# Optimization experiments

Measured on AMD Instinct MI355X. Metric: run time of the kernel, lower is better.

The kernel has to match this reference:

```python
import jax, jax.numpy as jnp
import numpy as np

B = 4            # batch size (max batch index + 1, fixed by construction)
H, W = 176, 200  # feature_map_size; x in [0,H), y in [0,W)
C_IN, C_OUT = 128, 256
BW, N = 4096, 64
EPS = 1e-5       # torch LayerNorm default


def setup_inputs() -> dict:
    key = jax.random.key(0)
    k1, k2, k3, k4, k5, k6, k7 = jax.random.split(key, 7)
    window_features = jax.random.normal(k1, (BW, N, C_IN), jnp.float32)
    bidx = jax.random.randint(k2, (BW, N, 1), 0, B)
    xidx = jax.random.randint(k3, (BW, N, 1), -8, H + 8)   # includes invalid coords
    yidx = jax.random.randint(k4, (BW, N, 1), -8, W + 8)
    window_indices = jnp.concatenate([bidx, xidx, yidx], axis=-1).astype(jnp.int32)
    norm_weight = 1.0 + 0.1 * jax.random.normal(k5, (C_IN,), jnp.float32)
    norm_bias = 0.1 * jax.random.normal(k6, (C_IN,), jnp.float32)
    lin_weight = jax.random.normal(k7, (C_OUT, C_IN), jnp.float32) / np.sqrt(C_IN)
    return {"window_features": window_features, "window_indices": window_indices,
            "norm_weight": norm_weight, "norm_bias": norm_bias, "lin_weight": lin_weight}


def reference(window_features, window_indices, norm_weight, norm_bias, lin_weight):
    # window_features: (BW, N, C_IN); window_indices: (BW, N, 3) = (batch, x, y)
    bw, n, c = window_features.shape
    feats = window_features.reshape(-1, c)                # (P, C)
    idx = window_indices.reshape(-1, 3)
    b, x, y = idx[:, 0], idx[:, 1], idx[:, 2]
    valid = (x >= 0) & (x < H) & (y >= 0) & (y < W)

    # unique + index_add_ + sparse-to-dense == scatter-add into dense BEV grid.
    # Invalid rows are routed out-of-bounds and dropped.
    bs = jnp.where(valid, b, B)
    xs = jnp.where(valid, x, 0)
    ys = jnp.where(valid, y, 0)
    # dense layout matches spconv: spatial_shape=[W, H], indices (b, y, x)
    dense_sum = jnp.zeros((B, W, H, c), window_features.dtype)
    dense_sum = dense_sum.at[bs, ys, xs].add(feats, mode="drop")
    count = jnp.zeros((B, W, H), window_features.dtype)
    count = count.at[bs, ys, xs].add(1.0, mode="drop")
    occupied = count > 0                                   # cells holding a unique voxel

    # LayerNorm over C (patch_norm=True) then Linear (bias=False) on occupied cells
    mu = jnp.mean(dense_sum, axis=-1, keepdims=True)
    var = jnp.mean(jnp.square(dense_sum - mu), axis=-1, keepdims=True)
    normed = (dense_sum - mu) * jax.lax.rsqrt(var + EPS) * norm_weight + norm_bias
    dense_out = jnp.einsum("bwhc,oc->bwho", normed, lin_weight)
    dense_out = jnp.where(occupied[..., None], dense_out, 0.0)  # empty cells stay zero

    # gather_operation: pull dense features back to each valid window point
    gathered = dense_out[jnp.where(valid, b, 0), ys, xs]   # (P, C_OUT)
    new_feats = jnp.where(valid[:, None], gathered, 0.0).reshape(bw, n, C_OUT)
    return new_feats, window_indices
```

## Files before the change

kernel.cpp:

```cpp
#include <hip/hip_runtime.h>
#include <stdint.h>

#define HH 176
#define WW 200
#define BB 4
#define CIN 128
#define COUT 256
#define NPTS (4096 * 64)
#define CELLS (BB * WW * HH)
#define FEAT_OUT_ELEMS ((size_t)NPTS * COUT)
#define CAP 32
#define LDSW16 260
#define FLATCAP 1024

typedef __attribute__((ext_vector_type(8))) short bf16x8;
typedef __attribute__((ext_vector_type(4))) float f32x4;

__device__ __forceinline__ unsigned short f2bf(float f) {
    union { float f; unsigned int u; } c; c.f = f;
    unsigned int u = c.u;
    u += 0x7fffu + ((u >> 16) & 1u);
    return (unsigned short)(u >> 16);
}
__device__ __forceinline__ float bf2f(unsigned int h16) {
    union { unsigned int u; float f; } c; c.u = h16 << 16;
    return c.f;
}

__global__ __launch_bounds__(256) void build_kernel(
    const int* __restrict__ idx, int* __restrict__ counts, int* __restrict__ plist,
    float* __restrict__ out_idx, float* __restrict__ out_feats)
{
    __shared__ unsigned char validf[256];
    int tid = threadIdx.x;
    int p0 = blockIdx.x * 256;
    int p = p0 + tid;
    int b = idx[3 * p], x = idx[3 * p + 1], y = idx[3 * p + 2];
    out_idx[3 * p]     = (float)b;
    out_idx[3 * p + 1] = (float)x;
    out_idx[3 * p + 2] = (float)y;
    bool valid = ((unsigned)x < HH && (unsigned)y < WW);
    validf[tid] = valid ? 1 : 0;
    if (valid) {
        int cell = (b * WW + y) * HH + x;
        int slot = atomicAdd(&counts[cell], 1);
        if (slot < CAP) plist[(size_t)cell * CAP + slot] = p;
    }
    __syncthreads();
    int w = tid >> 6, lane = tid & 63;
    float4 z = { 0.0f, 0.0f, 0.0f, 0.0f };
    for (int v = w; v < 256; v += 4)
        if (!validf[v])
            *(float4*)(out_feats + (size_t)(p0 + v) * COUT + lane * 4) = z;
}

__global__ __launch_bounds__(256) void cell_kernel(
    const float* __restrict__ feats, const int* __restrict__ counts,
    const int* __restrict__ plist,
    const float* __restrict__ nw, const float* __restrict__ nb,
    unsigned short* __restrict__ normed)
{
    int cell = blockIdx.x * 4 + (threadIdx.x >> 6);
    int lane = threadIdx.x & 63;
    int n = counts[cell]; n = n < CAP ? n : CAP;
    const int* pl = plist + (size_t)cell * CAP;
    float a0 = 0.0f, a1 = 0.0f;
    for (int i = 0; i < n; ++i) {
        int pid = pl[i];
        float2 v = *(const float2*)(feats + (size_t)pid * CIN + lane * 2);
        a0 += v.x; a1 += v.y;
    }
    float s = a0 + a1;
    float ss = a0 * a0 + a1 * a1;
    #pragma unroll
    for (int m = 32; m >= 1; m >>= 1) {
        s  += __shfl_xor(s, m, 64);
        ss += __shfl_xor(ss, m, 64);
    }
    float mu  = s * (1.0f / 128.0f);
    float var = ss * (1.0f / 128.0f) - mu * mu;
    float inv = rsqrtf(var + 1e-5f);
    float w0 = nw[lane * 2], w1 = nw[lane * 2 + 1];
    float b0 = nb[lane * 2], b1 = nb[lane * 2 + 1];
    ushort2 st;
    st.x = f2bf((a0 - mu) * inv * w0 + b0);
    st.y = f2bf((a1 - mu) * inv * w1 + b1);
    *(ushort2*)(normed + (size_t)cell * CIN + lane * 2) = st;
}

__global__ __launch_bounds__(256) void wcvt_kernel(
    const float* __restrict__ lw, unsigned short* __restrict__ wb)
{
    int i = blockIdx.x * 256 + threadIdx.x;
    wb[i] = f2bf(lw[i]);
}

__global__ __launch_bounds__(256) void gemm_scatter_kernel(
    const unsigned short* __restrict__ A,
    const unsigned short* __restrict__ Wb,
    const int* __restrict__ counts,
    const int* __restrict__ plist,
    float* __restrict__ out)
{
    __shared__ unsigned short lds16[64 * LDSW16];
    __shared__ int fpid[FLATCAP];
    __shared__ unsigned char fcell[FLATCAP];
    __shared__ int nflat;

    int n0 = blockIdx.x * 64;
    int tid = threadIdx.x;
    int w = tid >> 6;
    int lane = tid & 63;
    int l15 = lane & 15;
    int kgrp = (lane >> 4) * 8;
    int orow = (lane >> 4) * 4;

    if (tid == 0) nflat = 0;
    __syncthreads();

    if (tid < 64) {
        int cnt = counts[n0 + tid]; cnt = cnt < CAP ? cnt : CAP;
        if (cnt > 0) {
            int base = atomicAdd(&nflat, cnt);
            for (int s = 0; s < cnt; ++s) {
                int pos = base + s;
                if (pos < FLATCAP) {
                    fpid[pos] = plist[(size_t)(n0 + tid) * CAP + s];
                    fcell[pos] = (unsigned char)tid;
                }
            }
        }
    }

    bf16x8 a[4][4];
    #pragma unroll
    for (int i = 0; i < 4; ++i)
        #pragma unroll
        for (int kk = 0; kk < 4; ++kk)
            a[i][kk] = *(const bf16x8*)(Wb + (size_t)(((w * 4 + i) * 16 + l15) * CIN) + kgrp + kk * 32);

    const unsigned short* bbase = A + (size_t)(n0 + l15) * CIN + kgrp;

    #pragma unroll
    for (int j = 0; j < 4; ++j) {
        bf16x8 bb[4];
        #pragma unroll
        for (int kk = 0; kk < 4; ++kk)
            bb[kk] = *(const bf16x8*)(bbase + (size_t)j * 16 * CIN + kk * 32);

        f32x4 acc[4];
        #pragma unroll
        for (int i = 0; i < 4; ++i) acc[i] = (f32x4){0.0f, 0.0f, 0.0f, 0.0f};
        #pragma unroll
        for (int kk = 0; kk < 4; ++kk)
            #pragma unroll
            for (int i = 0; i < 4; ++i)
                acc[i] = __builtin_amdgcn_mfma_f32_16x16x32_bf16(a[i][kk], bb[kk], acc[i], 0, 0, 0);

        #pragma unroll
        for (int i = 0; i < 4; ++i) {
            int o = (w * 4 + i) * 16 + orow;
            ushort4 st;
            st.x = f2bf(acc[i][0]);
            st.y = f2bf(acc[i][1]);
            st.z = f2bf(acc[i][2]);
            st.w = f2bf(acc[i][3]);
            *(ushort4*)(&lds16[(j * 16 + l15) * LDSW16 + o]) = st;
        }
    }

    __syncthreads();

    int nt = nflat; nt = nt < FLATCAP ? nt : FLATCAP;
    for (int k = w; k < nt; k += 4) {
        int pid = fpid[k];
        int c = fcell[k];
        ushort4 v = *(const ushort4*)(&lds16[c * LDSW16 + lane * 4]);
        float4 o4;
        o4.x = bf2f(v.x);
        o4.y = bf2f(v.y);
        o4.z = bf2f(v.z);
        o4.w = bf2f(v.w);
        *(float4*)(out + (size_t)pid * COUT + lane * 4) = o4;
    }
}

extern "C" void kernel_launch(void* const* d_in, const int* in_sizes, int n_in,
                              void* d_out, int out_size, void* d_ws, size_t ws_size,
                              hipStream_t stream)
{
    const float* feats = (const float*)d_in[0];
    const int*   idx   = (const int*)d_in[1];
    const float* nw    = (const float*)d_in[2];
    const float* nb    = (const float*)d_in[3];
    const float* lw    = (const float*)d_in[4];
    float* out = (float*)d_out;

    char* ws = (char*)d_ws;
    int* counts = (int*)ws;
    int* plist  = (int*)(ws + (1u << 20));
    unsigned short* normed = (unsigned short*)(ws + (20u << 20));
    unsigned short* wb     = (unsigned short*)(ws + (60u << 20));

    hipMemsetAsync(counts, 0, (size_t)CELLS * 4, stream);
    build_kernel<<<NPTS / 256, 256, 0, stream>>>(idx, counts, plist, out + FEAT_OUT_ELEMS, out);
    cell_kernel<<<CELLS / 4, 256, 0, stream>>>(feats, counts, plist, nw, nb, normed);
    wcvt_kernel<<<COUT * CIN / 256, 256, 0, stream>>>(lw, wb);
    gemm_scatter_kernel<<<CELLS / 64, 256, 0, stream>>>(normed, wb, counts, plist, out);
}
```

Measured before the change: 478.2 us.

## Fuse per-cell accumulation and LayerNorm into GEMM-scatter kernel with LDS staging

```diff
diff --git a/kernel.cpp b/kernel.cpp
--- a/kernel.cpp
+++ b/kernel.cpp
@@ -10,6 +10,8 @@
 #define CELLS (BB * WW * HH)
 #define FEAT_OUT_ELEMS ((size_t)NPTS * COUT)
 #define CAP 32
+#define TCELLS 32
+#define LDSWF 132
 #define LDSW16 260
 #define FLATCAP 1024
 
@@ -25,6 +27,15 @@
 __device__ __forceinline__ float bf2f(unsigned int h16) {
     union { unsigned int u; float f; } c; c.u = h16 << 16;
     return c.f;
+}
+
+__global__ __launch_bounds__(256) void prep_kernel(
+    const float* __restrict__ lw, unsigned short* __restrict__ wb,
+    int* __restrict__ counts)
+{
+    int i = blockIdx.x * 256 + threadIdx.x;
+    if (i < COUT * CIN) wb[i] = f2bf(lw[i]);
+    counts[i] = 0;
 }
 
 __global__ __launch_bounds__(256) void build_kernel(
@@ -54,81 +65,68 @@
             *(float4*)(out_feats + (size_t)(p0 + v) * COUT + lane * 4) = z;
 }
 
-__global__ __launch_bounds__(256) void cell_kernel(
-    const float* __restrict__ feats, const int* __restrict__ counts,
-    const int* __restrict__ plist,
-    const float* __restrict__ nw, const float* __restrict__ nb,
-    unsigned short* __restrict__ normed)
-{
-    int cell = blockIdx.x * 4 + (threadIdx.x >> 6);
-    int lane = threadIdx.x & 63;
-    int n = counts[cell]; n = n < CAP ? n : CAP;
-    const int* pl = plist + (size_t)cell * CAP;
-    float a0 = 0.0f, a1 = 0.0f;
-    for (int i = 0; i < n; ++i) {
-        int pid = pl[i];
-        float2 v = *(const float2*)(feats + (size_t)pid * CIN + lane * 2);
-        a0 += v.x; a1 += v.y;
-    }
-    float s = a0 + a1;
-    float ss = a0 * a0 + a1 * a1;
-    #pragma unroll
-    for (int m = 32; m >= 1; m >>= 1) {
-        s  += __shfl_xor(s, m, 64);
-        ss += __shfl_xor(ss, m, 64);
-    }
-    float mu  = s * (1.0f / 128.0f);
-    float var = ss * (1.0f / 128.0f) - mu * mu;
-    float inv = rsqrtf(var + 1e-5f);
-    float w0 = nw[lane * 2], w1 = nw[lane * 2 + 1];
-    float b0 = nb[lane * 2], b1 = nb[lane * 2 + 1];
-    ushort2 st;
-    st.x = f2bf((a0 - mu) * inv * w0 + b0);
-    st.y = f2bf((a1 - mu) * inv * w1 + b1);
-    *(ushort2*)(normed + (size_t)cell * CIN + lane * 2) = st;
-}
-
-__global__ __launch_bounds__(256) void wcvt_kernel(
-    const float* __restrict__ lw, unsigned short* __restrict__ wb)
-{
-    int i = blockIdx.x * 256 + threadIdx.x;
-    wb[i] = f2bf(lw[i]);
-}
-
-__global__ __launch_bounds__(256) void gemm_scatter_kernel(
-    const unsigned short* __restrict__ A,
+__global__ __launch_bounds__(256) void fused_kernel(
+    const float* __restrict__ feats,
     const unsigned short* __restrict__ Wb,
     const int* __restrict__ counts,
     const int* __restrict__ plist,
+    const float* __restrict__ nw, const float* __restrict__ nb,
     float* __restrict__ out)
 {
-    __shared__ unsigned short lds16[64 * LDSW16];
+    __shared__ float accf[TCELLS * LDSWF];
+    __shared__ unsigned short normedl[TCELLS * LDSWF];
     __shared__ int fpid[FLATCAP];
     __shared__ unsigned char fcell[FLATCAP];
+    __shared__ int scnt[TCELLS];
     __shared__ int nflat;
-
-    int n0 = blockIdx.x * 64;
+    unsigned short* out16 = (unsigned short*)accf;
+
     int tid = threadIdx.x;
-    int w = tid >> 6;
-    int lane = tid & 63;
-    int l15 = lane & 15;
-    int kgrp = (lane >> 4) * 8;
-    int orow = (lane >> 4) * 4;
+    int w = tid >> 6, lane = tid & 63;
+    int l15 = lane & 15, g = lane >> 4;
+    int kgrp = g * 8, orow = g * 4;
+    int c0 = blockIdx.x * TCELLS;
 
     if (tid == 0) nflat = 0;
-    __syncthreads();
-
-    if (tid < 64) {
-        int cnt = counts[n0 + tid]; cnt = cnt < CAP ? cnt : CAP;
+    if (tid < TCELLS) {
+        int cnt = counts[c0 + tid];
+        scnt[tid] = cnt < CAP ? cnt : CAP;
+    }
+    for (int i = tid; i < TCELLS * LDSWF; i += 256) accf[i] = 0.0f;
+    __syncthreads();
+
+    if (tid < TCELLS) {
+        int cnt = scnt[tid];
         if (cnt > 0) {
             int base = atomicAdd(&nflat, cnt);
             for (int s = 0; s < cnt; ++s) {
-                int pos = base + s;
-                if (pos < FLATCAP) {
-                    fpid[pos] = plist[(size_t)(n0 + tid) * CAP + s];
-                    fcell[pos] = (unsigned char)tid;
-                }
+                fpid[base + s] = plist[(size_t)(c0 + tid) * CAP + s];
+                fcell[base + s] = (unsigned char)tid;
             }
+        }
+    }
+    __syncthreads();
+    int nt = nflat;
+
+    {
+        int k = w;
+        float2 v0 = {0.0f, 0.0f};
+        int cc0 = 0;
+        if (k < nt) {
+            int pid = fpid[k]; cc0 = fcell[k];
+            v0 = *(const float2*)(feats + (size_t)pid * CIN + lane * 2);
+        }
+        while (k < nt) {
+            int kn = k + 4;
+            float2 v1 = {0.0f, 0.0f};
+            int cc1 = 0;
+            if (kn < nt) {
+                int pid = fpid[kn]; cc1 = fcell[kn];
+                v1 = *(const float2*)(feats + (size_t)pid * CIN + lane * 2);
+            }
+            atomicAdd(&accf[cc0 * LDSWF + lane * 2], v0.x);
+            atomicAdd(&accf[cc0 * LDSWF + lane * 2 + 1], v0.y);
+            k = kn; cc0 = cc1; v0 = v1;
         }
     }
 
@@ -139,15 +137,37 @@
         for (int kk = 0; kk < 4; ++kk)
             a[i][kk] = *(const bf16x8*)(Wb + (size_t)(((w * 4 + i) * 16 + l15) * CIN) + kgrp + kk * 32);
 
-    const unsigned short* bbase = A + (size_t)(n0 + l15) * CIN + kgrp;
+    float w0 = nw[lane * 2], w1 = nw[lane * 2 + 1];
+    float b0 = nb[lane * 2], b1 = nb[lane * 2 + 1];
+
+    __syncthreads();
+
+    for (int c = w; c < TCELLS; c += 4) {
+        float a0 = accf[c * LDSWF + lane * 2];
+        float a1 = accf[c * LDSWF + lane * 2 + 1];
+        float s = a0 + a1;
+        float ss = a0 * a0 + a1 * a1;
+        #pragma unroll
+        for (int m = 32; m >= 1; m >>= 1) {
+            s  += __shfl_xor(s, m, 64);
+            ss += __shfl_xor(ss, m, 64);
+        }
+        float mu  = s * (1.0f / 128.0f);
+        float var = ss * (1.0f / 128.0f) - mu * mu;
+        float inv = rsqrtf(var + 1e-5f);
+        ushort2 st;
+        st.x = f2bf((a0 - mu) * inv * w0 + b0);
+        st.y = f2bf((a1 - mu) * inv * w1 + b1);
+        *(ushort2*)(&normedl[c * LDSWF + lane * 2]) = st;
+    }
+    __syncthreads();
 
     #pragma unroll
-    for (int j = 0; j < 4; ++j) {
+    for (int tj = 0; tj < 2; ++tj) {
         bf16x8 bb[4];
         #pragma unroll
         for (int kk = 0; kk < 4; ++kk)
-            bb[kk] = *(const bf16x8*)(bbase + (size_t)j * 16 * CIN + kk * 32);
-
+            bb[kk] = *(const bf16x8*)(normedl + (tj * 16 + l15) * LDSWF + kgrp + kk * 32);
         f32x4 acc[4];
         #pragma unroll
         for (int i = 0; i < 4; ++i) acc[i] = (f32x4){0.0f, 0.0f, 0.0f, 0.0f};
@@ -156,26 +176,23 @@
             #pragma unroll
             for (int i = 0; i < 4; ++i)
                 acc[i] = __builtin_amdgcn_mfma_f32_16x16x32_bf16(a[i][kk], bb[kk], acc[i], 0, 0, 0);
-
         #pragma unroll
         for (int i = 0; i < 4; ++i) {
-            int o = (w * 4 + i) * 16 + orow;
+            int o = w * 64 + i * 16 + orow;
             ushort4 st;
             st.x = f2bf(acc[i][0]);
             st.y = f2bf(acc[i][1]);
             st.z = f2bf(acc[i][2]);
             st.w = f2bf(acc[i][3]);
-            *(ushort4*)(&lds16[(j * 16 + l15) * LDSW16 + o]) = st;
-        }
-    }
-
-    __syncthreads();
-
-    int nt = nflat; nt = nt < FLATCAP ? nt : FLATCAP;
+            *(ushort4*)(&out16[(tj * 16 + l15) * LDSW16 + o]) = st;
+        }
+    }
+    __syncthreads();
+
     for (int k = w; k < nt; k += 4) {
         int pid = fpid[k];
         int c = fcell[k];
-        ushort4 v = *(const ushort4*)(&lds16[c * LDSW16 + lane * 4]);
+        ushort4 v = *(const ushort4*)(&out16[c * LDSW16 + lane * 4]);
         float4 o4;
         o4.x = bf2f(v.x);
         o4.y = bf2f(v.y);
@@ -199,12 +216,9 @@
     char* ws = (char*)d_ws;
     int* counts = (int*)ws;
     int* plist  = (int*)(ws + (1u << 20));
-    unsigned short* normed = (unsigned short*)(ws + (20u << 20));
-    unsigned short* wb     = (unsigned short*)(ws + (60u << 20));
-
-    hipMemsetAsync(counts, 0, (size_t)CELLS * 4, stream);
+    unsigned short* wb     = (unsigned short*)(ws + (20u << 20));
+
+    prep_kernel<<<CELLS / 256, 256, 0, stream>>>(lw, wb, counts);
     build_kernel<<<NPTS / 256, 256, 0, stream>>>(idx, counts, plist, out + FEAT_OUT_ELEMS, out);
-    cell_kernel<<<CELLS / 4, 256, 0, stream>>>(feats, counts, plist, nw, nb, normed);
-    wcvt_kernel<<<COUT * CIN / 256, 256, 0, stream>>>(lw, wb);
-    gemm_scatter_kernel<<<CELLS / 64, 256, 0, stream>>>(normed, wb, counts, plist, out);
-}
+    fused_kernel<<<CELLS / TCELLS, 256, 0, stream>>>(feats, wb, counts, plist, nw, nb, out);
+}
```

New measurement: 540.6 us. 1.13x slower.
